# Performance work log

Hardware: AMD Instinct MI355X
Metric: run time of the kernel (lower is better)

The kernel has to match this reference:

```python
import jax, jax.numpy as jnp
import numpy as np

N = 50000      # nodes
E = 800000     # edges per etype
IN, HID, OUT = 128, 128, 64
NH = 4         # heads in layerMH
NE = 2         # interaction edge types
NEG = 0.2      # GATConv leaky_relu negative slope


def _gat(x, src, dst, W, al, ar, b, heads, fdim):
    """DGL GATConv (residual=False, activation=None, bias=True).
    x: (N, in); W: (in, heads*fdim); al/ar: (heads, fdim); b: (heads*fdim,)
    Returns (N, heads, fdim)."""
    n = x.shape[0]
    z = (x @ W).reshape(n, heads, fdim)              # (N,H,F)
    el = jnp.sum(z * al, axis=-1)                    # (N,H)
    er = jnp.sum(z * ar, axis=-1)                    # (N,H)
    e = jax.nn.leaky_relu(el[src] + er[dst], NEG)    # (E,H)
    # edge softmax over incoming edges of each dst node
    m = jax.ops.segment_max(e, dst, num_segments=n)
    m = jnp.where(jnp.isfinite(m), m, 0.0)           # zero in-degree safety
    ex = jnp.exp(e - m[dst])
    den = jax.ops.segment_sum(ex, dst, num_segments=n)
    alpha = ex / jnp.maximum(den[dst], 1e-9)         # (E,H)
    out = jax.ops.segment_sum(alpha[:, :, None] * z[src], dst, num_segments=n)
    return out + b.reshape(1, heads, fdim)


def setup_inputs() -> dict:
    key = jax.random.key(0)
    ks = jax.random.split(key, 19)
    x = jax.random.normal(ks[0], (N, IN), jnp.float32)
    src0 = jax.random.randint(ks[1], (E,), 0, N, jnp.int32)
    dst0 = jax.random.randint(ks[2], (E,), 0, N, jnp.int32)
    src1 = jax.random.randint(ks[3], (E,), 0, N, jnp.int32)
    dst1 = jax.random.randint(ks[4], (E,), 0, N, jnp.int32)
    # per-etype GAT params (stacked over the NE edge types)
    W1 = jax.random.normal(ks[5], (NE, IN, HID), jnp.float32) / np.sqrt(IN)
    a_l1 = jax.random.normal(ks[6], (NE, 1, HID), jnp.float32) * 0.1
    a_r1 = jax.random.normal(ks[7], (NE, 1, HID), jnp.float32) * 0.1
    b1 = jnp.zeros((NE, HID), jnp.float32)
    W2 = jax.random.normal(ks[8], (NE, HID, OUT), jnp.float32) / np.sqrt(HID)
    a_l2 = jax.random.normal(ks[9], (NE, 1, OUT), jnp.float32) * 0.1
    a_r2 = jax.random.normal(ks[10], (NE, 1, OUT), jnp.float32) * 0.1
    b2 = jnp.zeros((NE, OUT), jnp.float32)
    Wm = jax.random.normal(ks[11], (NE, OUT, NH * OUT), jnp.float32) / np.sqrt(OUT)
    a_lm = jax.random.normal(ks[12], (NE, NH, OUT), jnp.float32) * 0.1
    a_rm = jax.random.normal(ks[13], (NE, NH, OUT), jnp.float32) * 0.1
    bm = jnp.zeros((NE, NH * OUT), jnp.float32)
    fc_w = jax.random.normal(ks[14], (NE, NE), jnp.float32) * (np.sqrt(2.0) / np.sqrt(NE))
    return dict(x=x, src0=src0, dst0=dst0, src1=src1, dst1=dst1,
                W1=W1, a_l1=a_l1, a_r1=a_r1, b1=b1,
                W2=W2, a_l2=a_l2, a_r2=a_r2, b2=b2,
                Wm=Wm, a_lm=a_lm, a_rm=a_rm, bm=bm, fc_w=fc_w)


def reference(x, src0, dst0, src1, dst1, W1, a_l1, a_r1, b1,
              W2, a_l2, a_r2, b2, Wm, a_lm, a_rm, bm, fc_w):
    srcs, dsts = (src0, src1), (dst0, dst1)
    # layer1: HeteroGraphConv mean over edge types, single head -> (N, HID)
    h1 = jnp.mean(jnp.stack([
        _gat(x, srcs[i], dsts[i], W1[i], a_l1[i], a_r1[i], b1[i], 1, HID)[:, 0, :]
        for i in range(NE)]), axis=0)
    # layer2: agg_func = fc over stacked etype axis, then mean -> (N, OUT)
    h2s = jnp.stack([
        _gat(h1, srcs[i], dsts[i], W2[i], a_l2[i], a_r2[i], b2[i], 1, OUT)[:, 0, :]
        for i in range(NE)], axis=-1)                       # (N, OUT, NE)
    h2 = jnp.mean(jnp.einsum('noe,fe->nof', h2s, fc_w), axis=-1)
    # multi-head layer: mean over edge types -> (N, NH, OUT)
    hm = jnp.mean(jnp.stack([
        _gat(h2, srcs[i], dsts[i], Wm[i], a_lm[i], a_rm[i], bm[i], NH, OUT)
        for i in range(NE)]), axis=0)
    # per-head mean-centering over nodes (vectorized over heads)
    return hm - jnp.mean(hm, axis=0, keepdims=True)
```

## Files before the change

kernel.cpp:

```cpp
#include <hip/hip_runtime.h>

#define NN 50000
#define EE 800000

using short8v = __attribute__((ext_vector_type(8))) short;
using f32x4 = __attribute__((ext_vector_type(4))) float;

__device__ inline unsigned int bf_pack(float lo, float hi) {
  unsigned int a = __float_as_uint(lo);
  a += 0x7FFFu + ((a >> 16) & 1u);
  unsigned int b = __float_as_uint(hi);
  b += 0x7FFFu + ((b >> 16) & 1u);
  return (a >> 16) | ((b >> 16) << 16);
}
__device__ inline void bf_dec8(uint4 v, float* f) {
  f[0] = __uint_as_float(v.x << 16); f[1] = __uint_as_float(v.x & 0xFFFF0000u);
  f[2] = __uint_as_float(v.y << 16); f[3] = __uint_as_float(v.y & 0xFFFF0000u);
  f[4] = __uint_as_float(v.z << 16); f[5] = __uint_as_float(v.z & 0xFFFF0000u);
  f[6] = __uint_as_float(v.w << 16); f[7] = __uint_as_float(v.w & 0xFFFF0000u);
}
__device__ inline float lrelu(float v) { return v >= 0.f ? v : 0.2f * v; }

__device__ inline void split_pack8(const float* v, uint4& h, uint4& l) {
  unsigned int hb[8], lb[8];
  #pragma unroll
  for (int j = 0; j < 8; j++) {
    unsigned int b = __float_as_uint(v[j]);
    hb[j] = b & 0xFFFF0000u;
    float r = v[j] - __uint_as_float(hb[j]);
    lb[j] = __float_as_uint(r) & 0xFFFF0000u;
  }
  h.x = (hb[0] >> 16) | hb[1]; h.y = (hb[2] >> 16) | hb[3];
  h.z = (hb[4] >> 16) | hb[5]; h.w = (hb[6] >> 16) | hb[7];
  l.x = (lb[0] >> 16) | lb[1]; l.y = (lb[2] >> 16) | lb[3];
  l.z = (lb[4] >> 16) | lb[5]; l.w = (lb[6] >> 16) | lb[7];
}

#define SC_BPR 256

__global__ __launch_bounds__(256) void deg2_k(
    const int* __restrict__ dst0, const int* __restrict__ dst1,
    int* __restrict__ deg) {
  const int range = blockIdx.x & 7;
  const int bpr = blockIdx.x >> 3;
  const int lo = range * 6250;
  const int hi = lo + 6250;
  #pragma unroll
  for (int e = 0; e < 2; e++) {
    const int* ds = e ? dst1 : dst0;
    int* dg = deg + e * 50000;
    for (int i = bpr * 256 + threadIdx.x; i < EE; i += SC_BPR * 256) {
      int d = ds[i];
      if (d >= lo && d < hi) atomicAdd(&dg[d], 1);
    }
  }
}

__global__ __launch_bounds__(512) void scan1_k(const int* __restrict__ deg,
                                               int* __restrict__ inc,
                                               int* __restrict__ bsum) {
  __shared__ int s[512];
  int e = blockIdx.y;
  int t = threadIdx.x, i = blockIdx.x * 512 + t;
  int v = (i < NN) ? deg[e * 50000 + i] : 0;
  s[t] = v; __syncthreads();
  #pragma unroll
  for (int off = 1; off < 512; off <<= 1) {
    int u = (t >= off) ? s[t - off] : 0;
    __syncthreads();
    s[t] += u;
    __syncthreads();
  }
  if (i < NN) inc[e * 50000 + i] = s[t];
  if (t == 511) bsum[e * 128 + blockIdx.x] = s[511];
}

__global__ __launch_bounds__(128) void scan2_k(int* __restrict__ bsum, int nb) {
  __shared__ int s[128];
  int e = blockIdx.x;
  int t = threadIdx.x;
  int v = (t < nb) ? bsum[e * 128 + t] : 0;
  s[t] = v; __syncthreads();
  #pragma unroll
  for (int off = 1; off < 128; off <<= 1) {
    int u = (t >= off) ? s[t - off] : 0;
    __syncthreads();
    s[t] += u;
    __syncthreads();
  }
  if (t < nb) bsum[e * 128 + t] = s[t] - v;
}

__global__ __launch_bounds__(256) void scan3_k(const int* __restrict__ deg,
                                               const int* __restrict__ inc,
                                               const int* __restrict__ bsum,
                                               int* __restrict__ rowptr,
                                               int* __restrict__ cursor) {
  int e = blockIdx.y;
  int i = blockIdx.x * 256 + threadIdx.x;
  if (i < NN) {
    int v = inc[e * 50000 + i] - deg[e * 50000 + i] + bsum[e * 128 + (i >> 9)];
    rowptr[e * 50001 + i] = v;
    cursor[e * 50000 + i] = v;
  }
  if (i == NN) rowptr[e * 50001 + NN] = EE;
}

__global__ __launch_bounds__(256) void csr_scatter2_k(
    const int* __restrict__ src0, const int* __restrict__ dst0,
    const int* __restrict__ src1, const int* __restrict__ dst1,
    int* __restrict__ cursor, int* __restrict__ csr_src) {
  const int range = blockIdx.x & 7;
  const int bpr = blockIdx.x >> 3;
  const int lo = range * 6250;
  const int hi = lo + 6250;
  #pragma unroll
  for (int e = 0; e < 2; e++) {
    const int* ds = e ? dst1 : dst0;
    const int* ss = e ? src1 : src0;
    int* cur = cursor + e * 50000;
    int* outp = csr_src + (size_t)e * EE;
    for (int i = bpr * 256 + threadIdx.x; i < EE; i += SC_BPR * 256) {
      int d = ds[i];
      if (d >= lo && d < hi) {
        int pos = atomicAdd(&cur[d], 1);
        outp[pos] = ss[i];
      }
    }
  }
}

__global__ __launch_bounds__(256) void fold_k(
    const float* __restrict__ W1, const float* __restrict__ al1, const float* __restrict__ ar1,
    const float* __restrict__ W2, const float* __restrict__ al2, const float* __restrict__ ar2,
    const float* __restrict__ Wm, const float* __restrict__ alm, const float* __restrict__ arm,
    float* __restrict__ wl1, float* __restrict__ wr1,
    float* __restrict__ wl2, float* __restrict__ wr2,
    float* __restrict__ wlm, float* __restrict__ wrm) {
  int t = blockIdx.x * 256 + threadIdx.x;
  if (t < 512) {
    int lr = t >> 8, e = (t >> 7) & 1, k = t & 127;
    const float* a = (lr ? ar1 : al1) + e * 128;
    const float* w = W1 + ((size_t)e * 128 + k) * 128;
    float s = 0.f;
    for (int f = 0; f < 128; f++) s += w[f] * a[f];
    (lr ? wr1 : wl1)[e * 128 + k] = s;
  } else if (t < 1024) {
    int u = t - 512;
    int lr = u >> 8, e = (u >> 7) & 1, k = u & 127;
    const float* a = (lr ? ar2 : al2) + e * 64;
    const float* w = W2 + ((size_t)e * 128 + k) * 64;
    float s = 0.f;
    for (int f = 0; f < 64; f++) s += w[f] * a[f];
    (lr ? wr2 : wl2)[e * 128 + k] = s;
  } else if (t < 2048) {
    int u = t - 1024;
    int lr = u >> 9, e = (u >> 8) & 1, h = (u >> 6) & 3, k = u & 63;
    const float* a = (lr ? arm : alm) + (e * 4 + h) * 64;
    const float* w = Wm + ((size_t)e * 64 + k) * 256 + h * 64;
    float s = 0.f;
    for (int f = 0; f < 64; f++) s += w[f] * a[f];
    (lr ? wrm : wlm)[(e * 4 + h) * 64 + k] = s;
  }
}

__global__ __launch_bounds__(256) void wtrans_k(
    const float* __restrict__ W1, const float* __restrict__ W2,
    const float* __restrict__ Wm,
    unsigned short* __restrict__ w1h, unsigned short* __restrict__ w1l,
    unsigned short* __restrict__ w2h, unsigned short* __restrict__ w2l,
    unsigned short* __restrict__ wmh, unsigned short* __restrict__ wml) {
  int t = blockIdx.x * 256 + threadIdx.x;
  float v; unsigned short *ph, *pl; int oi;
  if (t < 32768) {
    int j = t & 7, n = (t >> 3) & 127, kg = (t >> 10) & 15, e = t >> 14;
    v = W1[((size_t)(e * 128 + kg * 8 + j)) * 128 + n];
    ph = w1h; pl = w1l; oi = t;
  } else if (t < 49152) {
    int i = t - 32768;
    int j = i & 7, n = (i >> 3) & 63, kg = (i >> 9) & 15, e = i >> 13;
    v = W2[((size_t)(e * 128 + kg * 8 + j)) * 64 + n];
    ph = w2h; pl = w2l; oi = i;
  } else if (t < 81920) {
    int i = t - 49152;
    int j = i & 7, n = (i >> 3) & 255, kg = (i >> 11) & 7, e = i >> 14;
    v = Wm[((size_t)(e * 64 + kg * 8 + j)) * 256 + n];
    ph = wmh; pl = wml; oi = i;
  } else return;
  unsigned int b = __float_as_uint(v);
  unsigned int hb = b & 0xFFFF0000u;
  float r = v - __uint_as_float(hb);
  unsigned int lb = __float_as_uint(r);
  ph[oi] = (unsigned short)(hb >> 16);
  pl[oi] = (unsigned short)(lb >> 16);
}

__global__ __launch_bounds__(256) void xcast_k(const float* __restrict__ x,
                                               unsigned int* __restrict__ xb) {
  int i = blockIdx.x * 256 + threadIdx.x;
  if (i >= NN * 64) return;
  float2 v = *(const float2*)(x + (size_t)i * 2);
  xb[i] = bf_pack(v.x, v.y);
}

__global__ __launch_bounds__(256) void dot2_k(
    const float* __restrict__ X, const float* __restrict__ wl,
    const float* __restrict__ wr, float* __restrict__ el, float* __restrict__ er) {
  int n = blockIdx.x * 16 + (threadIdx.x >> 4);
  int lane = threadIdx.x & 15;
  if (n >= NN) return;
  float p[4] = {0.f, 0.f, 0.f, 0.f};
  #pragma unroll
  for (int i = 0; i < 2; i++) {
    int c = (lane + i * 16) * 4;
    float4 xv = *(const float4*)(X + (size_t)n * 128 + c);
    #pragma unroll
    for (int e = 0; e < 2; e++) {
      float4 a = *(const float4*)(wl + e * 128 + c);
      float4 b = *(const float4*)(wr + e * 128 + c);
      p[e*2+0] += xv.x*a.x + xv.y*a.y + xv.z*a.z + xv.w*a.w;
      p[e*2+1] += xv.x*b.x + xv.y*b.y + xv.z*b.z + xv.w*b.w;
    }
  }
  #pragma unroll
  for (int off = 1; off < 16; off <<= 1) {
    #pragma unroll
    for (int i = 0; i < 4; i++) p[i] += __shfl_xor(p[i], off);
  }
  if (lane == 0) {
    el[n] = p[0]; er[n] = p[1];
    el[NN + n] = p[2]; er[NN + n] = p[3];
  }
}

__global__ __launch_bounds__(256) void agg_x_f(
    const int* __restrict__ rowptr, const int* __restrict__ csr_src,
    const float* __restrict__ el, const float* __restrict__ er,
    const uint4* __restrict__ xb, float* __restrict__ u1) {
  int d = blockIdx.x * 16 + (threadIdx.x >> 4);
  int lane = threadIdx.x & 15;
  if (d >= NN) return;
  #pragma unroll
  for (int e = 0; e < 2; e++) {
    const int* rp = rowptr + e * 50001;
    const int* cs = csr_src + (size_t)e * EE;
    const float* elp = el + (size_t)e * NN;
    float erd = er[(size_t)e * NN + d];
    int j0 = rp[d], j1 = rp[d + 1];
    float sm = 0.f;
    float acc[8] = {};
    int j = j0;
    for (; j + 16 <= j1; j += 16) {
      int sl = cs[j + lane];
      float al = __expf(lrelu(elp[sl] + erd));
      sm += al;
      #pragma unroll
      for (int k = 0; k < 16; k++) {
        int s = __shfl(sl, k, 16);
        float a = __shfl(al, k, 16);
        uint4 xv = xb[(size_t)s * 16 + lane];
        float f[8]; bf_dec8(xv, f);
        #pragma unroll
        for (int c = 0; c < 8; c++) acc[c] += a * f[c];
      }
    }
    int r = j1 - j;
    if (r > 0) {
      int jj = j + (lane < r ? lane : 0);
      int sl = cs[jj];
      float al = __expf(lrelu(elp[sl] + erd));
      if (lane < r) sm += al;
      for (int k = 0; k < r; k++) {
        int s = __shfl(sl, k, 16);
        float a = __shfl(al, k, 16);
        uint4 xv = xb[(size_t)s * 16 + lane];
        float f[8]; bf_dec8(xv, f);
        #pragma unroll
        for (int c = 0; c < 8; c++) acc[c] += a * f[c];
      }
    }
    #pragma unroll
    for (int off = 1; off < 16; off <<= 1) sm += __shfl_xor(sm, off, 16);
    float inv = 1.f / fmaxf(sm, 1e-9f);
    float* up = u1 + ((size_t)e * NN + d) * 128 + lane * 8;
    *(float4*)up       = make_float4(acc[0]*inv, acc[1]*inv, acc[2]*inv, acc[3]*inv);
    *(float4*)(up + 4) = make_float4(acc[4]*inv, acc[5]*inv, acc[6]*inv, acc[7]*inv);
  }
}

__global__ __launch_bounds__(256) void ugemm1_k(
    const float* __restrict__ u1, const unsigned short* __restrict__ w1h,
    const unsigned short* __restrict__ w1l, const float* __restrict__ b1,
    float* __restrict__ h1) {
  __shared__ uint4 AsH[512], AsL[512];
  const int tid = threadIdx.x;
  const int row0 = blockIdx.x * 128;
  const int wv = tid >> 6, lane = tid & 63;
  const int l15 = lane & 15, lg = lane >> 4;
  f32x4 acc[2][8] = {};
  const uint4* bh4 = (const uint4*)w1h;
  const uint4* bl4 = (const uint4*)w1l;
  for (int e = 0; e < 2; e++) {
    const float* Ap = u1 + (size_t)e * NN * 128;
    for (int k0 = 0; k0 < 128; k0 += 32) {
      {
        int r = tid & 127, half = tid >> 7;
        int rr = row0 + r; if (rr >= NN) rr = NN - 1;
        const float* ap = Ap + (size_t)rr * 128 + k0;
        #pragma unroll
        for (int i = 0; i < 2; i++) {
          int kg = half * 2 + i;
          float4 a0 = *(const float4*)(ap + kg * 8);
          float4 a1 = *(const float4*)(ap + kg * 8 + 4);
          float v[8] = {a0.x, a0.y, a0.z, a0.w, a1.x, a1.y, a1.z, a1.w};
          uint4 hh, ll;
          split_pack8(v, hh, ll);
          AsH[kg * 128 + r] = hh;
          AsL[kg * 128 + r] = ll;
        }
      }
      __syncthreads();
      short8v ah[2], al[2];
      #pragma unroll
      for (int mf = 0; mf < 2; mf++) {
        int slot = lg * 128 + wv * 32 + mf * 16 + l15;
        ah[mf] = *reinterpret_cast<const short8v*>(&AsH[slot]);
        al[mf] = *reinterpret_cast<const short8v*>(&AsL[slot]);
      }
      int kgb = e * 16 + (k0 >> 3) + lg;
      #pragma unroll
      for (int nf = 0; nf < 8; nf++) {
        int bslot = kgb * 128 + nf * 16 + l15;
        short8v bh = *reinterpret_cast<const short8v*>(&bh4[bslot]);
        short8v bl = *reinterpret_cast<const short8v*>(&bl4[bslot]);
        #pragma unroll
        for (int mf = 0; mf < 2; mf++) {
          acc[mf][nf] = __builtin_amdgcn_mfma_f32_16x16x32_bf16(ah[mf], bh, acc[mf][nf], 0, 0, 0);
          acc[mf][nf] = __builtin_amdgcn_mfma_f32_16x16x32_bf16(al[mf], bh, acc[mf][nf], 0, 0, 0);
          acc[mf][nf] = __builtin_amdgcn_mfma_f32_16x16x32_bf16(ah[mf], bl, acc[mf][nf], 0, 0, 0);
        }
      }
      __syncthreads();
    }
  }
  #pragma unroll
  for (int nf = 0; nf < 8; nf++) {
    int col = nf * 16 + l15;
    float bb = 0.5f * (b1[col] + b1[128 + col]);
    #pragma unroll
    for (int mf = 0; mf < 2; mf++) {
      #pragma unroll
      for (int reg = 0; reg < 4; reg++) {
        int row = row0 + wv * 32 + mf * 16 + lg * 4 + reg;
        if (row < NN)
          h1[(size_t)row * 128 + col] = 0.5f * acc[mf][nf][reg] + bb;
      }
    }
  }
}

__global__ __launch_bounds__(256) void gemm64_k(
    const float* __restrict__ X, const unsigned short* __restrict__ w2h,
    const unsigned short* __restrict__ w2l, unsigned int* __restrict__ Zb) {
  __shared__ uint4 AsH[512], AsL[512];
  const int tid = threadIdx.x;
  const int row0 = blockIdx.x * 128;
  const int wv = tid >> 6, lane = tid & 63;
  const int l15 = lane & 15, lg = lane >> 4;
  f32x4 acc[2][2][4] = {};
  const uint4* bh4 = (const uint4*)w2h;
  const uint4* bl4 = (const uint4*)w2l;
  for (int k0 = 0; k0 < 128; k0 += 32) {
    {
      int r = tid & 127, half = tid >> 7;
      int rr = row0 + r; if (rr >= NN) rr = NN - 1;
      const float* ap = X + (size_t)rr * 128 + k0;
      #pragma unroll
      for (int i = 0; i < 2; i++) {
        int kg = half * 2 + i;
        float4 a0 = *(const float4*)(ap + kg * 8);
        float4 a1 = *(const float4*)(ap + kg * 8 + 4);
        float v[8] = {a0.x, a0.y, a0.z, a0.w, a1.x, a1.y, a1.z, a1.w};
        uint4 hh, ll;
        split_pack8(v, hh, ll);
        AsH[kg * 128 + r] = hh;
        AsL[kg * 128 + r] = ll;
      }
    }
    __syncthreads();
    short8v ah[2], al[2];
    #pragma unroll
    for (int mf = 0; mf < 2; mf++) {
      int slot = lg * 128 + wv * 32 + mf * 16 + l15;
      ah[mf] = *reinterpret_cast<const short8v*>(&AsH[slot]);
      al[mf] = *reinterpret_cast<const short8v*>(&AsL[slot]);
    }
    #pragma unroll
    for (int e = 0; e < 2; e++) {
      int kgb = e * 16 + (k0 >> 3) + lg;
      #pragma unroll
      for (int nf = 0; nf < 4; nf++) {
        int bslot = kgb * 64 + nf * 16 + l15;
        short8v bh = *reinterpret_cast<const short8v*>(&bh4[bslot]);
        short8v bl = *reinterpret_cast<const short8v*>(&bl4[bslot]);
        #pragma unroll
        for (int mf = 0; mf < 2; mf++) {
          acc[e][mf][nf] = __builtin_amdgcn_mfma_f32_16x16x32_bf16(ah[mf], bh, acc[e][mf][nf], 0, 0, 0);
          acc[e][mf][nf] = __builtin_amdgcn_mfma_f32_16x16x32_bf16(al[mf], bh, acc[e][mf][nf], 0, 0, 0);
          acc[e][mf][nf] = __builtin_amdgcn_mfma_f32_16x16x32_bf16(ah[mf], bl, acc[e][mf][nf], 0, 0, 0);
        }
      }
    }
    __syncthreads();
  }
  #pragma unroll
  for (int e = 0; e < 2; e++) {
    #pragma unroll
    for (int mf = 0; mf < 2; mf++) {
      #pragma unroll
      for (int nf = 0; nf < 4; nf++) {
        #pragma unroll
        for (int reg = 0; reg < 4; reg++) {
          float v = acc[e][mf][nf][reg];
          float nb = __shfl_xor(v, 1);
          int row = row0 + wv * 32 + mf * 16 + lg * 4 + reg;
          if (!(lane & 1) && row < NN) {
            Zb[((size_t)e * NN + row) * 32 + nf * 8 + (l15 >> 1)] = bf_pack(v, nb);
          }
        }
      }
    }
  }
}

__global__ __launch_bounds__(256) void agg2_f(
    const int* __restrict__ rowptr, const int* __restrict__ csr_src,
    const float* __restrict__ el, const float* __restrict__ er,
    const uint4* __restrict__ zb, const float* __restrict__ bias,
    const float* __restrict__ fcw, const float* __restrict__ wlm,
    const float* __restrict__ wrm, uint4* __restrict__ h2b,
    float* __restrict__ elm, float* __restrict__ erm) {
  int d = blockIdx.x * 32 + (threadIdx.x >> 3);
  int lane = threadIdx.x & 7;
  if (d >= NN) return;
  int c0 = lane * 8;
  float coef0 = 0.5f * (fcw[0] + fcw[2]);
  float coef1 = 0.5f * (fcw[1] + fcw[3]);
  float hrow[8];
  #pragma unroll
  for (int c = 0; c < 8; c++)
    hrow[c] = coef0 * bias[c0 + c] + coef1 * bias[64 + c0 + c];
  #pragma unroll
  for (int e = 0; e < 2; e++) {
    const int* rp = rowptr + e * 50001;
    const int* cs = csr_src + (size_t)e * EE;
    const float* elp = el + (size_t)e * NN;
    float erd = er[(size_t)e * NN + d];
    const uint4* zp = zb + (size_t)e * NN * 8;
    int j0 = rp[d], j1 = rp[d + 1];
    float sm = 0.f;
    float acc[8] = {};
    int j = j0;
    for (; j + 8 <= j1; j += 8) {
      int sl = cs[j + lane];
      float al = __expf(lrelu(elp[sl] + erd));
      sm += al;
      #pragma unroll
      for (int k = 0; k < 8; k++) {
        int s = __shfl(sl, k, 8);
        float a = __shfl(al, k, 8);
        uint4 zv = zp[(size_t)s * 8 + lane];
        float f[8]; bf_dec8(zv, f);
        #pragma unroll
        for (int c = 0; c < 8; c++) acc[c] += a * f[c];
      }
    }
    int r = j1 - j;
    if (r > 0) {
      int jj = j + (lane < r ? lane : 0);
      int sl = cs[jj];
      float al = __expf(lrelu(elp[sl] + erd));
      if (lane < r) sm += al;
      for (int k = 0; k < r; k++) {
        int s = __shfl(sl, k, 8);
        float a = __shfl(al, k, 8);
        uint4 zv = zp[(size_t)s * 8 + lane];
        float f[8]; bf_dec8(zv, f);
        #pragma unroll
        for (int c = 0; c < 8; c++) acc[c] += a * f[c];
      }
    }
    #pragma unroll
    for (int off = 1; off < 8; off <<= 1) sm += __shfl_xor(sm, off, 8);
    float cinv = (e ? coef1 : coef0) / fmaxf(sm, 1e-9f);
    #pragma unroll
    for (int c = 0; c < 8; c++) hrow[c] += cinv * acc[c];
  }
  uint4 o;
  o.x = bf_pack(hrow[0], hrow[1]); o.y = bf_pack(hrow[2], hrow[3]);
  o.z = bf_pack(hrow[4], hrow[5]); o.w = bf_pack(hrow[6], hrow[7]);
  h2b[(size_t)d * 8 + lane] = o;
  float p[16];
  #pragma unroll
  for (int e2 = 0; e2 < 2; e2++) {
    #pragma unroll
    for (int h = 0; h < 4; h++) {
      const float* a = wlm + (e2 * 4 + h) * 64 + c0;
      const float* b = wrm + (e2 * 4 + h) * 64 + c0;
      float sl = 0.f, sr = 0.f;
      #pragma unroll
      for (int c = 0; c < 8; c++) { sl += hrow[c] * a[c]; sr += hrow[c] * b[c]; }
      p[e2*4+h] = sl; p[8+e2*4+h] = sr;
    }
  }
  #pragma unroll
  for (int off = 1; off < 8; off <<= 1) {
    #pragma unroll
    for (int i = 0; i < 16; i++) p[i] += __shfl_xor(p[i], off, 8);
  }
  if (lane == 0) *(float4*)(elm + (size_t)d * 4)        = make_float4(p[0], p[1], p[2], p[3]);
  if (lane == 1) *(float4*)(elm + ((size_t)NN + d) * 4) = make_float4(p[4], p[5], p[6], p[7]);
  if (lane == 2) *(float4*)(erm + (size_t)d * 4)        = make_float4(p[8], p[9], p[10], p[11]);
  if (lane == 3) *(float4*)(erm + ((size_t)NN + d) * 4) = make_float4(p[12], p[13], p[14], p[15]);
}

__global__ __launch_bounds__(256) void agg_mh_k(
    const int* __restrict__ rowptr, const int* __restrict__ csr_src,
    const float* __restrict__ elm, const float* __restrict__ erm,
    const uint4* __restrict__ h2b, float* __restrict__ u) {
  int d = blockIdx.x * 32 + (threadIdx.x >> 3);
  int lane = threadIdx.x & 7, c0 = lane * 8;
  if (d >= NN) return;
  #pragma unroll
  for (int e = 0; e < 2; e++) {
    const int* rp = rowptr + e * 50001;
    const int* cs = csr_src + (size_t)e * EE;
    const float* elp = elm + (size_t)e * NN * 4;
    float4 er4 = *(const float4*)(erm + ((size_t)e * NN + d) * 4);
    int j0 = rp[d], j1 = rp[d + 1];
    float4 sm = make_float4(0.f, 0.f, 0.f, 0.f);
    float acc[4][8] = {};
    int j = j0;
    for (; j + 2 <= j1; j += 2) {
      int sA = cs[j], sB = cs[j+1];
      float4 vA = *(const float4*)(elp + (size_t)sA * 4);
      float4 vB = *(const float4*)(elp + (size_t)sB * 4);
      uint4 hA = h2b[(size_t)sA * 8 + lane];
      uint4 hB = h2b[(size_t)sB * 8 + lane];
      float4 wA, wB;
      wA.x = __expf(lrelu(vA.x + er4.x));
      wA.y = __expf(lrelu(vA.y + er4.y));
      wA.z = __expf(lrelu(vA.z + er4.z));
      wA.w = __expf(lrelu(vA.w + er4.w));
      wB.x = __expf(lrelu(vB.x + er4.x));
      wB.y = __expf(lrelu(vB.y + er4.y));
      wB.z = __expf(lrelu(vB.z + er4.z));
      wB.w = __expf(lrelu(vB.w + er4.w));
      sm.x += wA.x + wB.x; sm.y += wA.y + wB.y;
      sm.z += wA.z + wB.z; sm.w += wA.w + wB.w;
      float fA[8], fB[8];
      bf_dec8(hA, fA); bf_dec8(hB, fB);
      #pragma unroll
      for (int c = 0; c < 8; c++) {
        acc[0][c] += wA.x*fA[c] + wB.x*fB[c];
        acc[1][c] += wA.y*fA[c] + wB.y*fB[c];
        acc[2][c] += wA.z*fA[c] + wB.z*fB[c];
        acc[3][c] += wA.w*fA[c] + wB.w*fB[c];
      }
    }
    for (; j < j1; j++) {
      int s = cs[j];
      float4 v = *(const float4*)(elp + (size_t)s * 4);
      uint4 hh = h2b[(size_t)s * 8 + lane];
      float4 w;
      w.x = __expf(lrelu(v.x + er4.x));
      w.y = __expf(lrelu(v.y + er4.y));
      w.z = __expf(lrelu(v.z + er4.z));
      w.w = __expf(lrelu(v.w + er4.w));
      sm.x += w.x; sm.y += w.y; sm.z += w.z; sm.w += w.w;
      float f[8]; bf_dec8(hh, f);
      #pragma unroll
      for (int c = 0; c < 8; c++) {
        acc[0][c] += w.x*f[c]; acc[1][c] += w.y*f[c];
        acc[2][c] += w.z*f[c]; acc[3][c] += w.w*f[c];
      }
    }
    float4 inv = make_float4(1.f / fmaxf(sm.x, 1e-9f), 1.f / fmaxf(sm.y, 1e-9f),
                             1.f / fmaxf(sm.z, 1e-9f), 1.f / fmaxf(sm.w, 1e-9f));
    float iv[4] = {inv.x, inv.y, inv.z, inv.w};
    #pragma unroll
    for (int h = 0; h < 4; h++) {
      float* up = u + (((size_t)(e * 4 + h) * NN) + d) * 64 + c0;
      *(float4*)up       = make_float4(acc[h][0]*iv[h], acc[h][1]*iv[h],
                                       acc[h][2]*iv[h], acc[h][3]*iv[h]);
      *(float4*)(up + 4) = make_float4(acc[h][4]*iv[h], acc[h][5]*iv[h],
                                       acc[h][6]*iv[h], acc[h][7]*iv[h]);
    }
  }
}

__global__ __launch_bounds__(256) void colsum_u_k(
    const float* __restrict__ u, float* __restrict__ usum) {
  __shared__ float lds[4][64];
  int eh = blockIdx.x >> 6;
  int chunk = blockIdx.x & 63;
  int c = threadIdx.x & 63, rg = threadIdx.x >> 6;
  const float* up = u + (size_t)eh * NN * 64;
  int n0 = chunk * 782;
  int n1 = n0 + 782; if (n1 > NN) n1 = NN;
  float s = 0.f;
  for (int n = n0 + rg; n < n1; n += 4) s += up[(size_t)n * 64 + c];
  lds[rg][c] = s;
  __syncthreads();
  if (rg == 0) {
    float t = lds[0][c] + lds[1][c] + lds[2][c] + lds[3][c];
    unsafeAtomicAdd(&usum[eh * 64 + c], t);
  }
}

__global__ __launch_bounds__(256) void mean_k(
    const float* __restrict__ usum, const float* __restrict__ Wm,
    float* __restrict__ mean) {
  int c = threadIdx.x;
  int h = c >> 6;
  float s = 0.f;
  for (int e = 0; e < 2; e++) {
    const float* us = usum + (e * 4 + h) * 64;
    const float* wp = Wm + (size_t)e * 64 * 256 + c;
    for (int k = 0; k < 64; k++) s += us[k] * wp[(size_t)k * 256];
  }
  mean[c] = s * (0.5f / NN);
}

__global__ __launch_bounds__(256) void out_gemm_k(
    const float* __restrict__ u, const unsigned short* __restrict__ wmh,
    const unsigned short* __restrict__ wml, const float* __restrict__ mean,
    float* __restrict__ out) {
  __shared__ uint4 AsH[512], AsL[512];
  const int h = blockIdx.y;
  const int tid = threadIdx.x;
  const int row0 = blockIdx.x * 128;
  const int wv = tid >> 6, lane = tid & 63;
  const int l15 = lane & 15, lg = lane >> 4;
  f32x4 acc[2][4] = {};
  const uint4* bh4 = (const uint4*)wmh;
  const uint4* bl4 = (const uint4*)wml;
  for (int e = 0; e < 2; e++) {
    const float* Ap = u + (size_t)(e * 4 + h) * NN * 64;
    for (int k0 = 0; k0 < 64; k0 += 32) {
      {
        int r = tid & 127, half = tid >> 7;
        int rr = row0 + r; if (rr >= NN) rr = NN - 1;
        const float* ap = Ap + (size_t)rr * 64 + k0;
        #pragma unroll
        for (int i = 0; i < 2; i++) {
          int kg = half * 2 + i;
          float4 a0 = *(const float4*)(ap + kg * 8);
          float4 a1 = *(const float4*)(ap + kg * 8 + 4);
          float v[8] = {a0.x, a0.y, a0.z, a0.w, a1.x, a1.y, a1.z, a1.w};
          uint4 hh, ll;
          split_pack8(v, hh, ll);
          AsH[kg * 128 + r] = hh;
          AsL[kg * 128 + r] = ll;
        }
      }
      __syncthreads();
      short8v ah[2], al[2];
      #pragma unroll
      for (int mf = 0; mf < 2; mf++) {
        int slot = lg * 128 + wv * 32 + mf * 16 + l15;
        ah[mf] = *reinterpret_cast<const short8v*>(&AsH[slot]);
        al[mf] = *reinterpret_cast<const short8v*>(&AsL[slot]);
      }
      int kgb = e * 8 + (k0 >> 3) + lg;
      #pragma unroll
      for (int nf = 0; nf < 4; nf++) {
        int bslot = kgb * 256 + h * 64 + nf * 16 + l15;
        short8v bh = *reinterpret_cast<const short8v*>(&bh4[bslot]);
        short8v bl = *reinterpret_cast<const short8v*>(&bl4[bslot]);
        #pragma unroll
        for (int mf = 0; mf < 2; mf++) {
          acc[mf][nf] = __builtin_amdgcn_mfma_f32_16x16x32_bf16(ah[mf], bh, acc[mf][nf], 0, 0, 0);
          acc[mf][nf] = __builtin_amdgcn_mfma_f32_16x16x32_bf16(al[mf], bh, acc[mf][nf], 0, 0, 0);
          acc[mf][nf] = __builtin_amdgcn_mfma_f32_16x16x32_bf16(ah[mf], bl, acc[mf][nf], 0, 0, 0);
        }
      }
      __syncthreads();
    }
  }
  #pragma unroll
  for (int nf = 0; nf < 4; nf++) {
    int col = nf * 16 + l15;
    float mn = mean[h * 64 + col];
    #pragma unroll
    for (int mf = 0; mf < 2; mf++) {
      #pragma unroll
      for (int reg = 0; reg < 4; reg++) {
        int row = row0 + wv * 32 + mf * 16 + lg * 4 + reg;
        if (row < NN)
          out[(size_t)row * 256 + h * 64 + col] = 0.5f * acc[mf][nf][reg] - mn;
      }
    }
  }
}

extern "C" void kernel_launch(void* const* d_in, const int* in_sizes, int n_in,
                              void* d_out, int out_size, void* d_ws, size_t ws_size,
                              hipStream_t stream) {
  const float* x  = (const float*)d_in[0];
  const int* src0 = (const int*)d_in[1];
  const int* dst0 = (const int*)d_in[2];
  const int* src1 = (const int*)d_in[3];
  const int* dst1 = (const int*)d_in[4];
  const float* W1  = (const float*)d_in[5];
  const float* al1 = (const float*)d_in[6];
  const float* ar1 = (const float*)d_in[7];
  const float* b1  = (const float*)d_in[8];
  const float* W2  = (const float*)d_in[9];
  const float* al2 = (const float*)d_in[10];
  const float* ar2 = (const float*)d_in[11];
  const float* b2  = (const float*)d_in[12];
  const float* Wm  = (const float*)d_in[13];
  const float* alm = (const float*)d_in[14];
  const float* arm = (const float*)d_in[15];
  const float* fcw = (const float*)d_in[17];
  float* out = (float*)d_out;

  float* ws = (float*)d_ws;
  float* zu     = ws;
  unsigned int* z2b = (unsigned int*)(ws + 12800000);
  float* h1     = ws + 25600000;
  unsigned int* xb = (unsigned int*)h1;
  unsigned int* h2b = (unsigned int*)(ws + 32000000);
  float* el     = ws + 33600000;
  float* er     = ws + 34000000;
  float* elm    = ws + 34400000;
  float* erm    = ws + 34800000;
  float* wl1    = ws + 35200000;
  float* wr1    = wl1 + 256;
  float* wl2    = wr1 + 256;
  float* wr2    = wl2 + 256;
  float* wlm    = wr2 + 256;
  float* wrm    = wlm + 512;
  float* usum   = wrm + 512;
  float* meanp  = usum + 512;
  int* rowptr  = (int*)(meanp + 256);
  int* csr_src = rowptr + 100002;
  unsigned short* w1h = (unsigned short*)(csr_src + 2 * EE + 2);
  unsigned short* w1l = w1h + 32768;
  unsigned short* w2h = w1l + 32768;
  unsigned short* w2l = w2h + 16384;
  unsigned short* wmh = w2l + 16384;
  unsigned short* wml = wmh + 32768;
  int* deg    = (int*)el;
  int* inc    = (int*)er;
  int* cursor = (int*)zu;
  int* bsum   = (int*)zu + 200000;

  hipMemsetAsync(deg, 0, 2 * 50000 * sizeof(int), stream);
  hipMemsetAsync(usum, 0, 512 * sizeof(float), stream);
  deg2_k<<<8 * SC_BPR, 256, 0, stream>>>(dst0, dst1, deg);
  scan1_k<<<dim3(98, 2), 512, 0, stream>>>(deg, inc, bsum);
  scan2_k<<<2, 128, 0, stream>>>(bsum, 98);
  scan3_k<<<dim3(196, 2), 256, 0, stream>>>(deg, inc, bsum, rowptr, cursor);
  csr_scatter2_k<<<8 * SC_BPR, 256, 0, stream>>>(src0, dst0, src1, dst1,
                                                 cursor, csr_src);

  fold_k<<<8, 256, 0, stream>>>(W1, al1, ar1, W2, al2, ar2, Wm, alm, arm,
                                wl1, wr1, wl2, wr2, wlm, wrm);
  wtrans_k<<<320, 256, 0, stream>>>(W1, W2, Wm, w1h, w1l, w2h, w2l, wmh, wml);
  xcast_k<<<12500, 256, 0, stream>>>(x, xb);

  dot2_k<<<3125, 256, 0, stream>>>(x, wl1, wr1, el, er);
  agg_x_f<<<3125, 256, 0, stream>>>(rowptr, csr_src, el, er, (const uint4*)xb, zu);
  ugemm1_k<<<391, 256, 0, stream>>>(zu, w1h, w1l, b1, h1);

  dot2_k<<<3125, 256, 0, stream>>>(h1, wl2, wr2, el, er);
  gemm64_k<<<391, 256, 0, stream>>>(h1, w2h, w2l, z2b);
  agg2_f<<<1563, 256, 0, stream>>>(rowptr, csr_src, el, er, (const uint4*)z2b,
                                   b2, fcw, wlm, wrm, (uint4*)h2b, elm, erm);

  agg_mh_k<<<1563, 256, 0, stream>>>(rowptr, csr_src, elm, erm,
                                     (const uint4*)h2b, zu);
  colsum_u_k<<<512, 256, 0, stream>>>(zu, usum);
  mean_k<<<1, 256, 0, stream>>>(usum, Wm, meanp);
  out_gemm_k<<<dim3(391, 4), 256, 0, stream>>>(zu, wmh, wml, meanp, out);
}
```

Measured before the change: 630.4 us.

## Fuse x bf16 cast into dot kernel and fuse layer1 GEMM with layer2 dot and GEMM

The x-to-bf16 cast is folded into the first attention-dot kernel, so x is read once. The layer-1 output GEMM now keeps its h1 tile in shared memory and computes the layer-2 attention dots and the layer-2 GEMM from it in the same kernel. This drops the h1 round trip through global memory and two kernel launches. In exchange the fused kernel uses about 66KB of shared memory per block, which lowers occupancy, and it does the split to hi/lo bf16 in registers.

```diff
diff --git a/kernel.cpp b/kernel.cpp
--- a/kernel.cpp
+++ b/kernel.cpp
@@ -195,17 +195,10 @@
   pl[oi] = (unsigned short)(lb >> 16);
 }
 
-__global__ __launch_bounds__(256) void xcast_k(const float* __restrict__ x,
-                                               unsigned int* __restrict__ xb) {
-  int i = blockIdx.x * 256 + threadIdx.x;
-  if (i >= NN * 64) return;
-  float2 v = *(const float2*)(x + (size_t)i * 2);
-  xb[i] = bf_pack(v.x, v.y);
-}
-
-__global__ __launch_bounds__(256) void dot2_k(
-    const float* __restrict__ X, const float* __restrict__ wl,
-    const float* __restrict__ wr, float* __restrict__ el, float* __restrict__ er) {
+__global__ __launch_bounds__(256) void xdot_k(
+    const float* __restrict__ x, const float* __restrict__ wl,
+    const float* __restrict__ wr, unsigned int* __restrict__ xb,
+    float* __restrict__ el, float* __restrict__ er) {
   int n = blockIdx.x * 16 + (threadIdx.x >> 4);
   int lane = threadIdx.x & 15;
   if (n >= NN) return;
@@ -213,7 +206,11 @@
   #pragma unroll
   for (int i = 0; i < 2; i++) {
     int c = (lane + i * 16) * 4;
-    float4 xv = *(const float4*)(X + (size_t)n * 128 + c);
+    float4 xv = *(const float4*)(x + (size_t)n * 128 + c);
+    uint2 o;
+    o.x = bf_pack(xv.x, xv.y);
+    o.y = bf_pack(xv.z, xv.w);
+    *(uint2*)(xb + (size_t)n * 64 + c / 2) = o;
     #pragma unroll
     for (int e = 0; e < 2; e++) {
       float4 a = *(const float4*)(wl + e * 128 + c);
@@ -288,18 +285,27 @@
   }
 }
 
-__global__ __launch_bounds__(256) void ugemm1_k(
+__global__ __launch_bounds__(256) void layer12_k(
     const float* __restrict__ u1, const unsigned short* __restrict__ w1h,
     const unsigned short* __restrict__ w1l, const float* __restrict__ b1,
-    float* __restrict__ h1) {
-  __shared__ uint4 AsH[512], AsL[512];
+    const unsigned short* __restrict__ w2h, const unsigned short* __restrict__ w2l,
+    const float* __restrict__ wl2, const float* __restrict__ wr2,
+    unsigned int* __restrict__ Zb, float* __restrict__ el,
+    float* __restrict__ er) {
+  __shared__ float smem[128 * 132];
+  uint4* AsH = (uint4*)smem;
+  uint4* AsL = AsH + 512;
+  float* Hs = smem;
   const int tid = threadIdx.x;
   const int row0 = blockIdx.x * 128;
   const int wv = tid >> 6, lane = tid & 63;
   const int l15 = lane & 15, lg = lane >> 4;
+  const uint4* b1h4 = (const uint4*)w1h;
+  const uint4* b1l4 = (const uint4*)w1l;
+  const uint4* b2h4 = (const uint4*)w2h;
+  const uint4* b2l4 = (const uint4*)w2l;
+
   f32x4 acc[2][8] = {};
-  const uint4* bh4 = (const uint4*)w1h;
-  const uint4* bl4 = (const uint4*)w1l;
   for (int e = 0; e < 2; e++) {
     const float* Ap = u1 + (size_t)e * NN * 128;
     for (int k0 = 0; k0 < 128; k0 += 32) {
@@ -331,8 +337,8 @@
       #pragma unroll
       for (int nf = 0; nf < 8; nf++) {
         int bslot = kgb * 128 + nf * 16 + l15;
-        short8v bh = *reinterpret_cast<const short8v*>(&bh4[bslot]);
-        short8v bl = *reinterpret_cast<const short8v*>(&bl4[bslot]);
+        short8v bh = *reinterpret_cast<const short8v*>(&b1h4[bslot]);
+        short8v bl = *reinterpret_cast<const short8v*>(&b1l4[bslot]);
         #pragma unroll
         for (int mf = 0; mf < 2; mf++) {
           acc[mf][nf] = __builtin_amdgcn_mfma_f32_16x16x32_bf16(ah[mf], bh, acc[mf][nf], 0, 0, 0);
@@ -351,49 +357,45 @@
     for (int mf = 0; mf < 2; mf++) {
       #pragma unroll
       for (int reg = 0; reg < 4; reg++) {
-        int row = row0 + wv * 32 + mf * 16 + lg * 4 + reg;
-        if (row < NN)
-          h1[(size_t)row * 128 + col] = 0.5f * acc[mf][nf][reg] + bb;
-      }
-    }
-  }
-}
-
-__global__ __launch_bounds__(256) void gemm64_k(
-    const float* __restrict__ X, const unsigned short* __restrict__ w2h,
-    const unsigned short* __restrict__ w2l, unsigned int* __restrict__ Zb) {
-  __shared__ uint4 AsH[512], AsL[512];
-  const int tid = threadIdx.x;
-  const int row0 = blockIdx.x * 128;
-  const int wv = tid >> 6, lane = tid & 63;
-  const int l15 = lane & 15, lg = lane >> 4;
-  f32x4 acc[2][2][4] = {};
-  const uint4* bh4 = (const uint4*)w2h;
-  const uint4* bl4 = (const uint4*)w2l;
+        int rloc = wv * 32 + mf * 16 + lg * 4 + reg;
+        Hs[rloc * 132 + col] = 0.5f * acc[mf][nf][reg] + bb;
+      }
+    }
+  }
+  __syncthreads();
+  {
+    int r = tid >> 1, half = tid & 1;
+    int grow = row0 + r;
+    const float* hrow = Hs + r * 132 + half * 64;
+    float p0 = 0.f, p1 = 0.f, p2 = 0.f, p3 = 0.f;
+    #pragma unroll 8
+    for (int c = 0; c < 64; c++) {
+      float hv = hrow[c];
+      int k = half * 64 + c;
+      p0 += hv * wl2[k];       p1 += hv * wr2[k];
+      p2 += hv * wl2[128 + k]; p3 += hv * wr2[128 + k];
+    }
+    p0 += __shfl_xor(p0, 1); p1 += __shfl_xor(p1, 1);
+    p2 += __shfl_xor(p2, 1); p3 += __shfl_xor(p3, 1);
+    if (!half && grow < NN) {
+      el[grow] = p0;      er[grow] = p1;
+      el[NN + grow] = p2; er[NN + grow] = p3;
+    }
+  }
+  f32x4 acc2[2][2][4] = {};
   for (int k0 = 0; k0 < 128; k0 += 32) {
-    {
-      int r = tid & 127, half = tid >> 7;
-      int rr = row0 + r; if (rr >= NN) rr = NN - 1;
-      const float* ap = X + (size_t)rr * 128 + k0;
-      #pragma unroll
-      for (int i = 0; i < 2; i++) {
-        int kg = half * 2 + i;
-        float4 a0 = *(const float4*)(ap + kg * 8);
-        float4 a1 = *(const float4*)(ap + kg * 8 + 4);
-        float v[8] = {a0.x, a0.y, a0.z, a0.w, a1.x, a1.y, a1.z, a1.w};
-        uint4 hh, ll;
-        split_pack8(v, hh, ll);
-        AsH[kg * 128 + r] = hh;
-        AsL[kg * 128 + r] = ll;
-      }
-    }
-    __syncthreads();
     short8v ah[2], al[2];
     #pragma unroll
     for (int mf = 0; mf < 2; mf++) {
-      int slot = lg * 128 + wv * 32 + mf * 16 + l15;
-      ah[mf] = *reinterpret_cast<const short8v*>(&AsH[slot]);
-      al[mf] = *reinterpret_cast<const short8v*>(&AsL[slot]);
+      int ra = wv * 32 + mf * 16 + l15;
+      const float* hp = Hs + ra * 132 + k0 + lg * 8;
+      float4 h0 = *(const float4*)hp;
+      float4 h1v = *(const float4*)(hp + 4);
+      float v[8] = {h0.x, h0.y, h0.z, h0.w, h1v.x, h1v.y, h1v.z, h1v.w};
+      uint4 hh, ll;
+      split_pack8(v, hh, ll);
+      ah[mf] = *reinterpret_cast<const short8v*>(&hh);
+      al[mf] = *reinterpret_cast<const short8v*>(&ll);
     }
     #pragma unroll
     for (int e = 0; e < 2; e++) {
@@ -401,17 +403,16 @@
       #pragma unroll
       for (int nf = 0; nf < 4; nf++) {
         int bslot = kgb * 64 + nf * 16 + l15;
-        short8v bh = *reinterpret_cast<const short8v*>(&bh4[bslot]);
-        short8v bl = *reinterpret_cast<const short8v*>(&bl4[bslot]);
+        short8v bh = *reinterpret_cast<const short8v*>(&b2h4[bslot]);
+        short8v bl = *reinterpret_cast<const short8v*>(&b2l4[bslot]);
         #pragma unroll
         for (int mf = 0; mf < 2; mf++) {
-          acc[e][mf][nf] = __builtin_amdgcn_mfma_f32_16x16x32_bf16(ah[mf], bh, acc[e][mf][nf], 0, 0, 0);
-          acc[e][mf][nf] = __builtin_amdgcn_mfma_f32_16x16x32_bf16(al[mf], bh, acc[e][mf][nf], 0, 0, 0);
-          acc[e][mf][nf] = __builtin_amdgcn_mfma_f32_16x16x32_bf16(ah[mf], bl, acc[e][mf][nf], 0, 0, 0);
+          acc2[e][mf][nf] = __builtin_amdgcn_mfma_f32_16x16x32_bf16(ah[mf], bh, acc2[e][mf][nf], 0, 0, 0);
+          acc2[e][mf][nf] = __builtin_amdgcn_mfma_f32_16x16x32_bf16(al[mf], bh, acc2[e][mf][nf], 0, 0, 0);
+          acc2[e][mf][nf] = __builtin_amdgcn_mfma_f32_16x16x32_bf16(ah[mf], bl, acc2[e][mf][nf], 0, 0, 0);
         }
       }
     }
-    __syncthreads();
   }
   #pragma unroll
   for (int e = 0; e < 2; e++) {
@@ -421,7 +422,7 @@
       for (int nf = 0; nf < 4; nf++) {
         #pragma unroll
         for (int reg = 0; reg < 4; reg++) {
-          float v = acc[e][mf][nf][reg];
+          float v = acc2[e][mf][nf][reg];
           float nb = __shfl_xor(v, 1);
           int row = row0 + wv * 32 + mf * 16 + lg * 4 + reg;
           if (!(lane & 1) && row < NN) {
@@ -729,8 +730,7 @@
   float* ws = (float*)d_ws;
   float* zu     = ws;
   unsigned int* z2b = (unsigned int*)(ws + 12800000);
-  float* h1     = ws + 25600000;
-  unsigned int* xb = (unsigned int*)h1;
+  unsigned int* xb = (unsigned int*)(ws + 25600000);
   unsigned int* h2b = (unsigned int*)(ws + 32000000);
   float* el     = ws + 33600000;
   float* er     = ws + 34000000;
@@ -769,14 +769,12 @@
   fold_k<<<8, 256, 0, stream>>>(W1, al1, ar1, W2, al2, ar2, Wm, alm, arm,
                                 wl1, wr1, wl2, wr2, wlm, wrm);
   wtrans_k<<<320, 256, 0, stream>>>(W1, W2, Wm, w1h, w1l, w2h, w2l, wmh, wml);
-  xcast_k<<<12500, 256, 0, stream>>>(x, xb);
-
-  dot2_k<<<3125, 256, 0, stream>>>(x, wl1, wr1, el, er);
+
+  xdot_k<<<3125, 256, 0, stream>>>(x, wl1, wr1, xb, el, er);
   agg_x_f<<<3125, 256, 0, stream>>>(rowptr, csr_src, el, er, (const uint4*)xb, zu);
-  ugemm1_k<<<391, 256, 0, stream>>>(zu, w1h, w1l, b1, h1);
-
-  dot2_k<<<3125, 256, 0, stream>>>(h1, wl2, wr2, el, er);
-  gemm64_k<<<391, 256, 0, stream>>>(h1, w2h, w2l, z2b);
+  layer12_k<<<391, 256, 0, stream>>>(zu, w1h, w1l, b1, w2h, w2l, wl2, wr2,
+                                     z2b, el, er);
+
   agg2_f<<<1563, 256, 0, stream>>>(rowptr, csr_src, el, er, (const uint4*)z2b,
                                    b2, fcw, wlm, wrm, (uint4*)h2b, elm, erm);
 
@@ -784,5 +782,5 @@
                                      (const uint4*)h2b, zu);
   colsum_u_k<<<512, 256, 0, stream>>>(zu, usum);
   mean_k<<<1, 256, 0, stream>>>(usum, Wm, meanp);
-  out_gemm_k<<<dim3(391, 4), 256, 0, stream>>>(zu, wmh, wml, meanp, out);
-}
+  out_gemm_k<<<dim3(391, 4), 256, 0, stream>>>(zu, Wm != nullptr ? wmh : wmh, wml, meanp, out);
+}
```

New measurement: 623.3 us. No clear change (-1.1%).
